# Kernel tuning notes

Hardware: AMD Instinct MI355X
Metric: run time of the kernel (lower is better)

Reference implementation:

```python
import jax, jax.numpy as jnp
import numpy as np

TOPK = 60          # candidates kept per pyramid level
THRESH = 0.15      # score threshold
NMS_THRESH = 0.05  # IoU suppression threshold
NMS_TOPK = 20      # max boxes entering/leaving NMS per image
CROP = 128.0       # crop_size (cubic)
BATCH = 64
SIZES = (32, 16, 8)


def setup_inputs() -> dict:
    key = jax.random.key(0)
    ks = jax.random.split(key, 9)
    inp = {}
    for i, s in enumerate(SIZES):
        inp[f"cls{i}"] = jax.random.normal(ks[3 * i], (BATCH, 1, s, s, s), jnp.float32)
        inp[f"shape{i}"] = jax.random.uniform(ks[3 * i + 1], (BATCH, 3, s, s, s), jnp.float32)
        inp[f"offset{i}"] = jax.random.normal(ks[3 * i + 2], (BATCH, 3, s, s, s), jnp.float32)
    return inp


def _decode_level(cls, shp, off):
    """Anchor decode + sigmoid + per-level top-k (get_scores)."""
    B = cls.shape[0]
    D, H, W = cls.shape[2:]
    stride = jnp.asarray(CROP / D, cls.dtype)  # crop_size / feat_size
    ar = lambda n: jnp.arange(n, dtype=cls.dtype)
    zz, yy, xx = jnp.meshgrid(ar(D), ar(H), ar(W), indexing='ij')
    anchors = jnp.stack([zz, yy, xx], -1).reshape(-1, 3)          # [N,3] (z,y,x), grid_cell_offset=0
    scores = jax.nn.sigmoid(cls.reshape(B, -1))                    # [B,N]
    offs = off.reshape(B, 3, -1).transpose(0, 2, 1)                # [B,N,3]
    shps = shp.reshape(B, 3, -1).transpose(0, 2, 1)                # [B,N,3]
    ctr = (anchors[None] + offs) * stride                          # bbox_decode: center in input voxels
    bboxes = jnp.concatenate([ctr, shps], -1)                      # [B,N,6] = (z,y,x,d,h,w)
    ts, ti = jax.lax.top_k(scores, TOPK)
    return ts, ti, bboxes


def _pairwise_iou(b):
    """3D IoU for center-size boxes b: [K,6] = (z,y,x,d,h,w)."""
    c, s = b[:, :3], jnp.maximum(b[:, 3:], 0.0)
    lo, hi = c - 0.5 * s, c + 0.5 * s
    inter = jnp.prod(
        jnp.maximum(jnp.minimum(hi[:, None], hi[None]) - jnp.maximum(lo[:, None], lo[None]), 0.0), -1)
    vol = jnp.prod(s, -1)
    return inter / (vol[:, None] + vol[None] - inter + 1e-8)


def _nms_image(scores, boxes):
    """Threshold mask + greedy 3D NMS on top NMS_TOPK candidates; fixed-size output [M,8]."""
    M = scores.shape[0]
    valid = scores > THRESH
    s = jnp.where(valid, scores, -jnp.inf)
    order = jnp.argsort(-s)[:NMS_TOPK]                             # descending score, truncated to nms_topk
    s_k, b_k, v_k = s[order], boxes[order], valid[order]
    iou = jax.lax.stop_gradient(_pairwise_iou(b_k))                # suppression decisions are non-diff
    keep_list = [v_k[0]]
    for i in range(1, NMS_TOPK):                                   # small fixed unroll (20)
        prev = jnp.stack(keep_list)
        sup = jnp.any(prev & (iou[i, :i] > NMS_THRESH))
        keep_list.append(v_k[i] & ~sup)
    keep = jnp.stack(keep_list)                                    # [K] kept flags, in descending-score order
    rows = jnp.where(keep, jnp.cumsum(keep) - 1, M)                # compact kept boxes to the front; M -> dropped
    row_vals = jnp.concatenate(
        [jnp.ones((NMS_TOPK, 1), s_k.dtype), s_k[:, None], b_k], 1)  # [K,8] = (1, score, z,y,x,d,h,w)
    dets = -jnp.ones((M, 8), s_k.dtype)
    return dets.at[rows].set(row_vals, mode='drop')


def _forward(cls0, shape0, offset0, cls1, shape1, offset1, cls2, shape2, offset2):
    levels = [(cls0, shape0, offset0), (cls1, shape1, offset1), (cls2, shape2, offset2)]
    ts_l, ti_l, bb_l = [], [], []
    shift = 0
    for c, s, o in levels:
        ts, ti, bb = _decode_level(c, s, o)
        ti_l.append(ti + shift)
        shift += bb.shape[1]
        ts_l.append(ts)
        bb_l.append(bb)
    scores = jnp.concatenate(ts_l, 1)                              # [B, 3*TOPK]
    idx = jnp.concatenate(ti_l, 1)
    bboxes = jnp.concatenate(bb_l, 1)                              # [B, Ntot, 6]
    cand = jnp.take_along_axis(bboxes, idx[..., None], axis=1)     # [B, 3*TOPK, 6]
    return jax.vmap(_nms_image)(scores, cand)                      # [B, 3*TOPK, 8]


def reference(cls0, shape0, offset0, cls1, shape1, offset1, cls2, shape2, offset2):
    return _forward(cls0, shape0, offset0, cls1, shape1, offset1, cls2, shape2, offset2)
```

## Files before the change

### kernel.cpp

```cpp
#include <hip/hip_runtime.h>
#include <math.h>

#define BATCH 64
#define V0 32768
#define V1 4096
#define V2 512
#define NTOT 37376
#define K 20
#define M_OUT 180
#define NT 256

#define SLICES 32
#define SLICE4 292
#define CAP 16
#define NKEY 128
#define TLOG 3.0f

__device__ __forceinline__ unsigned long long make_key_lo(float logit, unsigned int lo ) {
    float s = 1.0f / (1.0f + expf(-logit));
    return ((unsigned long long)__float_as_uint(s) << 32) | (unsigned long long)lo;
}

#define INSERT(LV, GG) do {                                             \
    unsigned long long ck_ = make_key_lo((LV), ~(GG));                  \
    if (ck_ > keys[K-1]) {                                              \
        _Pragma("unroll")                                               \
        for (int j_ = 0; j_ < K; ++j_) {                                \
            if (ck_ > keys[j_]) {                                       \
                unsigned long long t_ = keys[j_]; keys[j_] = ck_; ck_ = t_; \
            }                                                           \
        }                                                               \
    }                                                                   \
} while (0)

__global__ __launch_bounds__(NT) void scan_kernel(
    const float* __restrict__ cls0, const float* __restrict__ cls1, const float* __restrict__ cls2,
    unsigned long long* __restrict__ wsKeys, int* __restrict__ wsCnt)
{
    const int blk = blockIdx.x;
    const int b = blk >> 5, s = blk & 31;
    const int tid = threadIdx.x;
    __shared__ int lcnt;
    if (tid == 0) lcnt = 0;
    __syncthreads();

    const int base4 = s * SLICE4;
    for (int i4 = tid; i4 < SLICE4; i4 += NT) {
        int f4 = base4 + i4;
        float4 v;
        if (f4 < V0 / 4)                 v = ((const float4*)(cls0 + (size_t)b * V0))[f4];
        else if (f4 < (V0 + V1) / 4)     v = ((const float4*)(cls1 + (size_t)b * V1))[f4 - V0 / 4];
        else                             v = ((const float4*)(cls2 + (size_t)b * V2))[f4 - (V0 + V1) / 4];
        unsigned int g = 4u * (unsigned int)f4;
        float a0 = v.x, a1 = v.y, a2 = v.z, a3 = v.w;
        float aa[4] = {a0, a1, a2, a3};
#pragma unroll
        for (int c = 0; c < 4; ++c) {
            if (aa[c] > TLOG) {
                int slot = atomicAdd(&lcnt, 1);
                if (slot < CAP)
                    wsKeys[(size_t)blk * CAP + slot] =
                        ((unsigned long long)__float_as_uint(aa[c]) << 32) |
                        (unsigned long long)(~(g + (unsigned int)c));
            }
        }
    }
    __syncthreads();
    if (tid == 0) wsCnt[blk] = lcnt;
}

__global__ __launch_bounds__(NT) void final_kernel(
    const float* __restrict__ cls0, const float* __restrict__ shp0, const float* __restrict__ off0,
    const float* __restrict__ cls1, const float* __restrict__ shp1, const float* __restrict__ off1,
    const float* __restrict__ cls2, const float* __restrict__ shp2, const float* __restrict__ off2,
    const unsigned long long* __restrict__ wsKeys, const int* __restrict__ wsCnt,
    float* __restrict__ out, int use_ws)
{
    const int b   = blockIdx.x;
    const int tid = threadIdx.x;

    __shared__ unsigned long long sKeys[NT * K];
    __shared__ unsigned long long lkeys[NKEY];
    __shared__ unsigned long long sorted[K];
    __shared__ int cnts[SLICES];
    __shared__ int pfx[SLICES];
    __shared__ int sDegen;
    __shared__ float sBox[K][6];
    __shared__ float sScore[K];
    __shared__ int   sValid[K];
    __shared__ float sIou[K * K];
    __shared__ int   sRow[K];

    if (use_ws && tid < SLICES) cnts[tid] = wsCnt[b * SLICES + tid];
    __syncthreads();
    if (tid == 0) {
        int dg = !use_ws, t = 0;
        if (use_ws) {
            for (int s = 0; s < SLICES; ++s) {
                pfx[s] = t;
                int c = cnts[s];
                if (c > CAP) dg = 1;
                t += c;
            }
            if (t < K || t > NKEY) dg = 1;
        }
        sDegen = dg;
    }
    __syncthreads();

    if (!sDegen) {
        for (int t = tid; t < NKEY; t += NT) lkeys[t] = 0ull;
        __syncthreads();
        for (int t = tid; t < SLICES * CAP; t += NT) {
            int s = t / CAP, i = t % CAP;
            if (i < cnts[s]) {
                unsigned long long pk = wsKeys[(size_t)(b * SLICES + s) * CAP + i];
                float logit = __uint_as_float((unsigned int)(pk >> 32));
                lkeys[pfx[s] + i] = make_key_lo(logit, (unsigned int)pk);
            }
        }
        __syncthreads();
        if (tid < NKEY) {
            unsigned long long my = lkeys[tid];
            int rank = 0;
#pragma unroll 8
            for (int i = 0; i < NKEY; ++i) rank += (lkeys[i] > my) ? 1 : 0;
            if (my != 0ull && rank < K) sorted[rank] = my;
        }
        __syncthreads();
    } else {
        unsigned long long keys[K];
#pragma unroll
        for (int j = 0; j < K; ++j) keys[j] = 0ull;
        {
            const float4* c0 = (const float4*)(cls0 + (size_t)b * V0);
#pragma unroll 1
            for (int it = 0; it < V0 / (4 * NT); ++it) {
                int i4 = tid + it * NT;
                float4 v = c0[i4];
                unsigned int g = 4u * (unsigned int)i4;
                INSERT(v.x, g); INSERT(v.y, g + 1); INSERT(v.z, g + 2); INSERT(v.w, g + 3);
            }
            const float4* c1 = (const float4*)(cls1 + (size_t)b * V1);
#pragma unroll 1
            for (int it = 0; it < V1 / (4 * NT); ++it) {
                int i4 = tid + it * NT;
                float4 v = c1[i4];
                unsigned int g = V0 + 4u * (unsigned int)i4;
                INSERT(v.x, g); INSERT(v.y, g + 1); INSERT(v.z, g + 2); INSERT(v.w, g + 3);
            }
            if (tid < V2 / 4) {
                const float4* c2 = (const float4*)(cls2 + (size_t)b * V2);
                float4 v = c2[tid];
                unsigned int g = V0 + V1 + 4u * (unsigned int)tid;
                INSERT(v.x, g); INSERT(v.y, g + 1); INSERT(v.z, g + 2); INSERT(v.w, g + 3);
            }
        }
#pragma unroll
        for (int j = 0; j < K; ++j) sKeys[tid * K + j] = keys[j];
        for (int half = NT / 2; half >= 1; half >>= 1) {
            __syncthreads();
            if (tid < half) {
                int aB = tid * K, bB = (tid + half) * K;
                unsigned long long ov[K];
                int ia = 0, ib = 0;
                unsigned long long av = sKeys[aB], bv = sKeys[bB];
#pragma unroll
                for (int p = 0; p < K; ++p) {
                    bool ta = (av >= bv);
                    ov[p] = ta ? av : bv;
                    if (ta) { ++ia; av = (ia < K) ? sKeys[aB + ia] : 0ull; }
                    else    { ++ib; bv = (ib < K) ? sKeys[bB + ib] : 0ull; }
                }
#pragma unroll
                for (int p = 0; p < K; ++p) sKeys[aB + p] = ov[p];
            }
        }
        __syncthreads();
        if (tid < K) sorted[tid] = sKeys[tid];
        __syncthreads();
    }

    if (tid < K) {
        unsigned long long key = sorted[tid];
        float score = __uint_as_float((unsigned int)(key >> 32));
        unsigned int g = ~((unsigned int)key);
        sScore[tid] = score;
        sValid[tid] = (score > 0.15f) ? 1 : 0;

        int v, D;
        const float* sp; const float* op;
        if (g < V0)           { v = (int)g;             D = 32; sp = shp0; op = off0; }
        else if (g < V0 + V1) { v = (int)(g - V0);      D = 16; sp = shp1; op = off1; }
        else                  { v = (int)(g - V0 - V1); D = 8;  sp = shp2; op = off2; }
        int Vl = D * D * D, HW = D * D;
        int z = v / HW, rem = v - z * HW, y = rem / D, x = rem - y * D;
        float stride = 128.0f / (float)D;
        const float* opb = op + (size_t)b * 3 * Vl;
        const float* spb = sp + (size_t)b * 3 * Vl;
        sBox[tid][0] = ((float)z + opb[v])          * stride;
        sBox[tid][1] = ((float)y + opb[Vl + v])     * stride;
        sBox[tid][2] = ((float)x + opb[2 * Vl + v]) * stride;
        sBox[tid][3] = spb[v];
        sBox[tid][4] = spb[Vl + v];
        sBox[tid][5] = spb[2 * Vl + v];
    }
    __syncthreads();

    for (int p = tid; p < K * K; p += NT) {
#pragma clang fp contract(off)
        int i = p / K, j = p % K;
        float ci0 = sBox[i][0], ci1 = sBox[i][1], ci2 = sBox[i][2];
        float si0 = fmaxf(sBox[i][3], 0.0f), si1 = fmaxf(sBox[i][4], 0.0f), si2 = fmaxf(sBox[i][5], 0.0f);
        float cj0 = sBox[j][0], cj1 = sBox[j][1], cj2 = sBox[j][2];
        float sj0 = fmaxf(sBox[j][3], 0.0f), sj1 = fmaxf(sBox[j][4], 0.0f), sj2 = fmaxf(sBox[j][5], 0.0f);
        float in0 = fmaxf(fminf(ci0 + 0.5f * si0, cj0 + 0.5f * sj0) - fmaxf(ci0 - 0.5f * si0, cj0 - 0.5f * sj0), 0.0f);
        float in1 = fmaxf(fminf(ci1 + 0.5f * si1, cj1 + 0.5f * sj1) - fmaxf(ci1 - 0.5f * si1, cj1 - 0.5f * sj1), 0.0f);
        float in2 = fmaxf(fminf(ci2 + 0.5f * si2, cj2 + 0.5f * sj2) - fmaxf(ci2 - 0.5f * si2, cj2 - 0.5f * sj2), 0.0f);
        float inter = in0 * in1 * in2;
        float voli = si0 * si1 * si2, volj = sj0 * sj1 * sj2;
        sIou[p] = inter / (voli + volj - inter + 1e-8f);
    }
    __syncthreads();

    if (tid == 0) {
        int keep[K];
        int cnt = 0;
#pragma unroll
        for (int i = 0; i < K; ++i) sRow[i] = -1;
        for (int i = 0; i < K; ++i) {
            int sup = 0;
            for (int j = 0; j < i; ++j)
                sup |= (keep[j] && (sIou[i * K + j] > 0.05f));
            keep[i] = sValid[i] && !sup;
            if (keep[i]) { sRow[cnt] = i; ++cnt; }
        }
    }
    __syncthreads();

    float* ob = out + (size_t)b * (M_OUT * 8);
    for (int e = tid; e < M_OUT * 8; e += NT) {
        int r = e >> 3, c = e & 7;
        float val = -1.0f;
        if (r < K) {
            int i = sRow[r];
            if (i >= 0) {
                if (c == 0)      val = 1.0f;
                else if (c == 1) val = sScore[i];
                else             val = sBox[i][c - 2];
            }
        }
        ob[e] = val;
    }
}

extern "C" void kernel_launch(void* const* d_in, const int* in_sizes, int n_in,
                              void* d_out, int out_size, void* d_ws, size_t ws_size,
                              hipStream_t stream) {
    const float* cls0 = (const float*)d_in[0];
    const float* shp0 = (const float*)d_in[1];
    const float* off0 = (const float*)d_in[2];
    const float* cls1 = (const float*)d_in[3];
    const float* shp1 = (const float*)d_in[4];
    const float* off1 = (const float*)d_in[5];
    const float* cls2 = (const float*)d_in[6];
    const float* shp2 = (const float*)d_in[7];
    const float* off2 = (const float*)d_in[8];
    float* out = (float*)d_out;

    const size_t keysBytes = (size_t)BATCH * SLICES * CAP * sizeof(unsigned long long);
    const size_t needBytes = keysBytes + (size_t)BATCH * SLICES * sizeof(int);

    if (ws_size >= needBytes) {
        unsigned long long* wsKeys = (unsigned long long*)d_ws;
        int* wsCnt = (int*)((char*)d_ws + keysBytes);
        scan_kernel<<<BATCH * SLICES, NT, 0, stream>>>(cls0, cls1, cls2, wsKeys, wsCnt);
        final_kernel<<<BATCH, NT, 0, stream>>>(cls0, shp0, off0, cls1, shp1, off1,
                                               cls2, shp2, off2, wsKeys, wsCnt, out, 1);
    } else {
        final_kernel<<<BATCH, NT, 0, stream>>>(cls0, shp0, off0, cls1, shp1, off1,
                                               cls2, shp2, off2, nullptr, nullptr, out, 0);
    }
}
```

Baseline: 113.3 us.

## Fuse scan and final stages via last-block-done atomic counter

Merges the per-slice threshold scan and the per-image selection/NMS kernel into one launch: each slice block bumps a per-image atomic counter, and the last block to finish performs the merge, decode and NMS. The degenerate full-scan fallback now picks the top-K by repeated block-wide max reduction instead of a shared-memory merge tree, which shrinks shared memory use. This removes one kernel launch and the gap between the two kernels, but adds a hipMemsetAsync, relies on acquire/release ordering of the workspace writes, and leaves the tail work on a single late block per image.

```diff
diff --git a/kernel.cpp b/kernel.cpp
--- a/kernel.cpp
+++ b/kernel.cpp
@@ -33,154 +33,67 @@
     }                                                                   \
 } while (0)
 
-__global__ __launch_bounds__(NT) void scan_kernel(
+__device__ void fullscan_select(
+    int b, int tid,
     const float* __restrict__ cls0, const float* __restrict__ cls1, const float* __restrict__ cls2,
-    unsigned long long* __restrict__ wsKeys, int* __restrict__ wsCnt)
+    unsigned long long* heads , unsigned long long* sorted )
 {
-    const int blk = blockIdx.x;
-    const int b = blk >> 5, s = blk & 31;
-    const int tid = threadIdx.x;
-    __shared__ int lcnt;
-    if (tid == 0) lcnt = 0;
-    __syncthreads();
-
-    const int base4 = s * SLICE4;
-    for (int i4 = tid; i4 < SLICE4; i4 += NT) {
-        int f4 = base4 + i4;
-        float4 v;
-        if (f4 < V0 / 4)                 v = ((const float4*)(cls0 + (size_t)b * V0))[f4];
-        else if (f4 < (V0 + V1) / 4)     v = ((const float4*)(cls1 + (size_t)b * V1))[f4 - V0 / 4];
-        else                             v = ((const float4*)(cls2 + (size_t)b * V2))[f4 - (V0 + V1) / 4];
-        unsigned int g = 4u * (unsigned int)f4;
-        float a0 = v.x, a1 = v.y, a2 = v.z, a3 = v.w;
-        float aa[4] = {a0, a1, a2, a3};
+    unsigned long long keys[K];
 #pragma unroll
-        for (int c = 0; c < 4; ++c) {
-            if (aa[c] > TLOG) {
-                int slot = atomicAdd(&lcnt, 1);
-                if (slot < CAP)
-                    wsKeys[(size_t)blk * CAP + slot] =
-                        ((unsigned long long)__float_as_uint(aa[c]) << 32) |
-                        (unsigned long long)(~(g + (unsigned int)c));
+    for (int j = 0; j < K; ++j) keys[j] = 0ull;
+    {
+        const float4* c0 = (const float4*)(cls0 + (size_t)b * V0);
+#pragma unroll 1
+        for (int it = 0; it < V0 / (4 * NT); ++it) {
+            int i4 = tid + it * NT;
+            float4 v = c0[i4];
+            unsigned int g = 4u * (unsigned int)i4;
+            INSERT(v.x, g); INSERT(v.y, g + 1); INSERT(v.z, g + 2); INSERT(v.w, g + 3);
+        }
+        const float4* c1 = (const float4*)(cls1 + (size_t)b * V1);
+#pragma unroll 1
+        for (int it = 0; it < V1 / (4 * NT); ++it) {
+            int i4 = tid + it * NT;
+            float4 v = c1[i4];
+            unsigned int g = V0 + 4u * (unsigned int)i4;
+            INSERT(v.x, g); INSERT(v.y, g + 1); INSERT(v.z, g + 2); INSERT(v.w, g + 3);
+        }
+        if (tid < V2 / 4) {
+            const float4* c2 = (const float4*)(cls2 + (size_t)b * V2);
+            float4 v = c2[tid];
+            unsigned int g = V0 + V1 + 4u * (unsigned int)tid;
+            INSERT(v.x, g); INSERT(v.y, g + 1); INSERT(v.z, g + 2); INSERT(v.w, g + 3);
+        }
+    }
+    int h = 0;
+    for (int r = 0; r < K; ++r) {
+        heads[tid] = (h < K) ? keys[h] : 0ull;
+        __syncthreads();
+        for (int off = NT / 2; off >= 1; off >>= 1) {
+            if (tid < off) {
+                unsigned long long o = heads[tid + off];
+                if (o > heads[tid]) heads[tid] = o;
             }
-        }
-    }
-    __syncthreads();
-    if (tid == 0) wsCnt[blk] = lcnt;
-}
-
-__global__ __launch_bounds__(NT) void final_kernel(
-    const float* __restrict__ cls0, const float* __restrict__ shp0, const float* __restrict__ off0,
-    const float* __restrict__ cls1, const float* __restrict__ shp1, const float* __restrict__ off1,
-    const float* __restrict__ cls2, const float* __restrict__ shp2, const float* __restrict__ off2,
-    const unsigned long long* __restrict__ wsKeys, const int* __restrict__ wsCnt,
-    float* __restrict__ out, int use_ws)
+            __syncthreads();
+        }
+        unsigned long long win = heads[0];
+        __syncthreads();
+        if (tid == 0) sorted[r] = win;
+        unsigned long long mine = (h < K) ? keys[h] : 0ull;
+        if (mine == win && win != 0ull) ++h;
+    }
+    __syncthreads();
+}
+
+__device__ void tail_process(
+    int b, int tid,
+    const float* __restrict__ shp0, const float* __restrict__ off0,
+    const float* __restrict__ shp1, const float* __restrict__ off1,
+    const float* __restrict__ shp2, const float* __restrict__ off2,
+    const unsigned long long* sorted ,
+    float (*sBox)[6], float* sScore, int* sValid, float* sIou, int* sRow,
+    float* __restrict__ out)
 {
-    const int b   = blockIdx.x;
-    const int tid = threadIdx.x;
-
-    __shared__ unsigned long long sKeys[NT * K];
-    __shared__ unsigned long long lkeys[NKEY];
-    __shared__ unsigned long long sorted[K];
-    __shared__ int cnts[SLICES];
-    __shared__ int pfx[SLICES];
-    __shared__ int sDegen;
-    __shared__ float sBox[K][6];
-    __shared__ float sScore[K];
-    __shared__ int   sValid[K];
-    __shared__ float sIou[K * K];
-    __shared__ int   sRow[K];
-
-    if (use_ws && tid < SLICES) cnts[tid] = wsCnt[b * SLICES + tid];
-    __syncthreads();
-    if (tid == 0) {
-        int dg = !use_ws, t = 0;
-        if (use_ws) {
-            for (int s = 0; s < SLICES; ++s) {
-                pfx[s] = t;
-                int c = cnts[s];
-                if (c > CAP) dg = 1;
-                t += c;
-            }
-            if (t < K || t > NKEY) dg = 1;
-        }
-        sDegen = dg;
-    }
-    __syncthreads();
-
-    if (!sDegen) {
-        for (int t = tid; t < NKEY; t += NT) lkeys[t] = 0ull;
-        __syncthreads();
-        for (int t = tid; t < SLICES * CAP; t += NT) {
-            int s = t / CAP, i = t % CAP;
-            if (i < cnts[s]) {
-                unsigned long long pk = wsKeys[(size_t)(b * SLICES + s) * CAP + i];
-                float logit = __uint_as_float((unsigned int)(pk >> 32));
-                lkeys[pfx[s] + i] = make_key_lo(logit, (unsigned int)pk);
-            }
-        }
-        __syncthreads();
-        if (tid < NKEY) {
-            unsigned long long my = lkeys[tid];
-            int rank = 0;
-#pragma unroll 8
-            for (int i = 0; i < NKEY; ++i) rank += (lkeys[i] > my) ? 1 : 0;
-            if (my != 0ull && rank < K) sorted[rank] = my;
-        }
-        __syncthreads();
-    } else {
-        unsigned long long keys[K];
-#pragma unroll
-        for (int j = 0; j < K; ++j) keys[j] = 0ull;
-        {
-            const float4* c0 = (const float4*)(cls0 + (size_t)b * V0);
-#pragma unroll 1
-            for (int it = 0; it < V0 / (4 * NT); ++it) {
-                int i4 = tid + it * NT;
-                float4 v = c0[i4];
-                unsigned int g = 4u * (unsigned int)i4;
-                INSERT(v.x, g); INSERT(v.y, g + 1); INSERT(v.z, g + 2); INSERT(v.w, g + 3);
-            }
-            const float4* c1 = (const float4*)(cls1 + (size_t)b * V1);
-#pragma unroll 1
-            for (int it = 0; it < V1 / (4 * NT); ++it) {
-                int i4 = tid + it * NT;
-                float4 v = c1[i4];
-                unsigned int g = V0 + 4u * (unsigned int)i4;
-                INSERT(v.x, g); INSERT(v.y, g + 1); INSERT(v.z, g + 2); INSERT(v.w, g + 3);
-            }
-            if (tid < V2 / 4) {
-                const float4* c2 = (const float4*)(cls2 + (size_t)b * V2);
-                float4 v = c2[tid];
-                unsigned int g = V0 + V1 + 4u * (unsigned int)tid;
-                INSERT(v.x, g); INSERT(v.y, g + 1); INSERT(v.z, g + 2); INSERT(v.w, g + 3);
-            }
-        }
-#pragma unroll
-        for (int j = 0; j < K; ++j) sKeys[tid * K + j] = keys[j];
-        for (int half = NT / 2; half >= 1; half >>= 1) {
-            __syncthreads();
-            if (tid < half) {
-                int aB = tid * K, bB = (tid + half) * K;
-                unsigned long long ov[K];
-                int ia = 0, ib = 0;
-                unsigned long long av = sKeys[aB], bv = sKeys[bB];
-#pragma unroll
-                for (int p = 0; p < K; ++p) {
-                    bool ta = (av >= bv);
-                    ov[p] = ta ? av : bv;
-                    if (ta) { ++ia; av = (ia < K) ? sKeys[aB + ia] : 0ull; }
-                    else    { ++ib; bv = (ib < K) ? sKeys[bB + ib] : 0ull; }
-                }
-#pragma unroll
-                for (int p = 0; p < K; ++p) sKeys[aB + p] = ov[p];
-            }
-        }
-        __syncthreads();
-        if (tid < K) sorted[tid] = sKeys[tid];
-        __syncthreads();
-    }
-
     if (tid < K) {
         unsigned long long key = sorted[tid];
         float score = __uint_as_float((unsigned int)(key >> 32));
@@ -254,6 +167,129 @@
     }
 }
 
+__global__ __launch_bounds__(NT) void fused_kernel(
+    const float* __restrict__ cls0, const float* __restrict__ shp0, const float* __restrict__ off0,
+    const float* __restrict__ cls1, const float* __restrict__ shp1, const float* __restrict__ off1,
+    const float* __restrict__ cls2, const float* __restrict__ shp2, const float* __restrict__ off2,
+    unsigned long long* __restrict__ wsKeys, int* __restrict__ wsCnt, int* __restrict__ done,
+    float* __restrict__ out)
+{
+    const int blk = blockIdx.x;
+    const int b = blk >> 5, s = blk & 31;
+    const int tid = threadIdx.x;
+
+    __shared__ int lcnt;
+    __shared__ int sLast;
+    __shared__ unsigned long long heads[NT];
+    __shared__ unsigned long long lkeys[NKEY];
+    __shared__ unsigned long long sorted[K];
+    __shared__ int cnts[SLICES];
+    __shared__ int pfx[SLICES];
+    __shared__ int sDegen;
+    __shared__ float sBox[K][6];
+    __shared__ float sScore[K];
+    __shared__ int   sValid[K];
+    __shared__ float sIou[K * K];
+    __shared__ int   sRow[K];
+
+    if (tid == 0) lcnt = 0;
+    __syncthreads();
+
+    const int base4 = s * SLICE4;
+    for (int i4 = tid; i4 < SLICE4; i4 += NT) {
+        int f4 = base4 + i4;
+        float4 v;
+        if (f4 < V0 / 4)             v = ((const float4*)(cls0 + (size_t)b * V0))[f4];
+        else if (f4 < (V0 + V1) / 4) v = ((const float4*)(cls1 + (size_t)b * V1))[f4 - V0 / 4];
+        else                         v = ((const float4*)(cls2 + (size_t)b * V2))[f4 - (V0 + V1) / 4];
+        unsigned int g = 4u * (unsigned int)f4;
+        float aa[4] = {v.x, v.y, v.z, v.w};
+#pragma unroll
+        for (int c = 0; c < 4; ++c) {
+            if (aa[c] > TLOG) {
+                int slot = atomicAdd(&lcnt, 1);
+                if (slot < CAP)
+                    wsKeys[(size_t)blk * CAP + slot] =
+                        ((unsigned long long)__float_as_uint(aa[c]) << 32) |
+                        (unsigned long long)(~(g + (unsigned int)c));
+            }
+        }
+    }
+    __syncthreads();
+
+    if (tid == 0) {
+        wsCnt[blk] = lcnt;
+        int old = __hip_atomic_fetch_add(&done[b], 1, __ATOMIC_ACQ_REL,
+                                         __HIP_MEMORY_SCOPE_AGENT);
+        sLast = (old == SLICES - 1) ? 1 : 0;
+    }
+    __syncthreads();
+    if (!sLast) return;
+
+    if (tid < SLICES) cnts[tid] = wsCnt[b * SLICES + tid];
+    __syncthreads();
+    if (tid == 0) {
+        int dg = 0, t = 0;
+        for (int q = 0; q < SLICES; ++q) {
+            pfx[q] = t;
+            int c = cnts[q];
+            if (c > CAP) dg = 1;
+            t += c;
+        }
+        if (t < K || t > NKEY) dg = 1;
+        sDegen = dg;
+    }
+    __syncthreads();
+
+    if (!sDegen) {
+        for (int t = tid; t < NKEY; t += NT) lkeys[t] = 0ull;
+        __syncthreads();
+        for (int t = tid; t < SLICES * CAP; t += NT) {
+            int q = t / CAP, i = t % CAP;
+            if (i < cnts[q]) {
+                unsigned long long pk = wsKeys[(size_t)(b * SLICES + q) * CAP + i];
+                float logit = __uint_as_float((unsigned int)(pk >> 32));
+                lkeys[pfx[q] + i] = make_key_lo(logit, (unsigned int)pk);
+            }
+        }
+        __syncthreads();
+        if (tid < NKEY) {
+            unsigned long long my = lkeys[tid];
+            int rank = 0;
+#pragma unroll 8
+            for (int i = 0; i < NKEY; ++i) rank += (lkeys[i] > my) ? 1 : 0;
+            if (my != 0ull && rank < K) sorted[rank] = my;
+        }
+        __syncthreads();
+    } else {
+        fullscan_select(b, tid, cls0, cls1, cls2, heads, sorted);
+    }
+
+    tail_process(b, tid, shp0, off0, shp1, off1, shp2, off2,
+                 sorted, sBox, sScore, sValid, sIou, sRow, out);
+}
+
+__global__ __launch_bounds__(NT) void exact_kernel(
+    const float* __restrict__ cls0, const float* __restrict__ shp0, const float* __restrict__ off0,
+    const float* __restrict__ cls1, const float* __restrict__ shp1, const float* __restrict__ off1,
+    const float* __restrict__ cls2, const float* __restrict__ shp2, const float* __restrict__ off2,
+    float* __restrict__ out)
+{
+    const int b = blockIdx.x;
+    const int tid = threadIdx.x;
+    __shared__ unsigned long long heads[NT];
+    __shared__ unsigned long long sorted[K];
+    __shared__ float sBox[K][6];
+    __shared__ float sScore[K];
+    __shared__ int   sValid[K];
+    __shared__ float sIou[K * K];
+    __shared__ int   sRow[K];
+
+    fullscan_select(b, tid, cls0, cls1, cls2, heads, sorted);
+    tail_process(b, tid, shp0, off0, shp1, off1, shp2, off2,
+                 sorted, sBox, sScore, sValid, sIou, sRow, out);
+}
+
 extern "C" void kernel_launch(void* const* d_in, const int* in_sizes, int n_in,
                               void* d_out, int out_size, void* d_ws, size_t ws_size,
                               hipStream_t stream) {
@@ -269,16 +305,20 @@
     float* out = (float*)d_out;
 
     const size_t keysBytes = (size_t)BATCH * SLICES * CAP * sizeof(unsigned long long);
-    const size_t needBytes = keysBytes + (size_t)BATCH * SLICES * sizeof(int);
+    const size_t cntBytes  = (size_t)BATCH * SLICES * sizeof(int);
+    const size_t doneBytes = (size_t)BATCH * sizeof(int);
+    const size_t needBytes = keysBytes + cntBytes + doneBytes;
 
     if (ws_size >= needBytes) {
         unsigned long long* wsKeys = (unsigned long long*)d_ws;
         int* wsCnt = (int*)((char*)d_ws + keysBytes);
-        scan_kernel<<<BATCH * SLICES, NT, 0, stream>>>(cls0, cls1, cls2, wsKeys, wsCnt);
-        final_kernel<<<BATCH, NT, 0, stream>>>(cls0, shp0, off0, cls1, shp1, off1,
-                                               cls2, shp2, off2, wsKeys, wsCnt, out, 1);
+        int* done  = (int*)((char*)d_ws + keysBytes + cntBytes);
+        hipMemsetAsync(done, 0, doneBytes, stream);
+        fused_kernel<<<BATCH * SLICES, NT, 0, stream>>>(
+            cls0, shp0, off0, cls1, shp1, off1, cls2, shp2, off2,
+            wsKeys, wsCnt, done, out);
     } else {
-        final_kernel<<<BATCH, NT, 0, stream>>>(cls0, shp0, off0, cls1, shp1, off1,
-                                               cls2, shp2, off2, nullptr, nullptr, out, 0);
-    }
-}
+        exact_kernel<<<BATCH, NT, 0, stream>>>(
+            cls0, shp0, off0, cls1, shp1, off1, cls2, shp2, off2, out);
+    }
+}
```

Result: slower. 172.2 us (+52.0%).
